# Performance work log

Measured on AMD Instinct MI355X. Metric: run time of the kernel, lower is better.

The kernel has to match this reference:

```python
import jax, jax.numpy as jnp
import numpy as np

B, H, VOCAB, STEPS = 256, 512, 100, 200  # TEXT_MAX_LEN - 1 = 200
SOS_IDX = 0  # char2idx['<SOS>'] == 0 (first entry of chars list)


def setup_inputs() -> dict:
    key = jax.random.key(0)
    ks = jax.random.split(key, 8)
    s = 0.05  # keep gates/tanh away from saturation, like trained-weight scale
    return {
        "feat": jax.random.normal(ks[0], (B, H), jnp.float32),          # resnet pooler_output
        "embed_table": jax.random.normal(ks[1], (VOCAB, H), jnp.float32) * s,
        "w_ih": jax.random.normal(ks[2], (3 * H, H), jnp.float32) * s,   # torch weight_ih_l0
        "w_hh": jax.random.normal(ks[3], (3 * H, H), jnp.float32) * s,   # torch weight_hh_l0
        "b_ih": jax.random.normal(ks[4], (3 * H,), jnp.float32) * s,
        "b_hh": jax.random.normal(ks[5], (3 * H,), jnp.float32) * s,
        "proj_w": jax.random.normal(ks[6], (VOCAB, H), jnp.float32) * s,
        "proj_b": jax.random.normal(ks[7], (VOCAB,), jnp.float32) * s,
    }


def _gru_cell(x, h, w_ih, w_hh, b_ih, b_hh):
    # torch GRU cell: gates ordered [r, z, n]
    gi = x @ w_ih.T + b_ih          # [B, 3H]
    gh = h @ w_hh.T + b_hh          # [B, 3H]
    i_r, i_z, i_n = jnp.split(gi, 3, axis=-1)
    h_r, h_z, h_n = jnp.split(gh, 3, axis=-1)
    r = jax.nn.sigmoid(i_r + h_r)
    z = jax.nn.sigmoid(i_z + h_z)
    n = jnp.tanh(i_n + r * h_n)
    return (1.0 - z) * n + z * h


def reference(feat, embed_table, w_ih, w_hh, b_ih, b_hh, proj_w, proj_b):
    batch = feat.shape[0]
    # hidden initialized from resnet features; first input = embed(<SOS>)
    h0 = feat                                             # [B, H]
    inp0 = jnp.broadcast_to(embed_table[SOS_IDX], (batch, H))

    def step(carry, _):
        inp, h = carry
        h_new = _gru_cell(inp, h, w_ih, w_hh, b_ih, b_hh)
        # GRU output == new hidden (1 layer); it is fed back as next input
        return (h_new, h_new), h_new

    _, outs = jax.lax.scan(step, (inp0, h0), None, length=STEPS)  # [T, B, H]
    res = jnp.transpose(outs, (1, 0, 2))                          # [B, T, H]
    logits = res @ proj_w.T + proj_b                              # [B, T, V]
    return jnp.transpose(logits, (0, 2, 1))                       # [B, V, T]
```

## Files before the change

kernel.cpp:

```cpp
#include <hip/hip_runtime.h>
#include <hip/hip_bf16.h>
#include <math.h>


typedef __bf16 bf16_t;
typedef __bf16 bf16x8 __attribute__((ext_vector_type(8)));
typedef float f32x4 __attribute__((ext_vector_type(4)));
typedef unsigned long long u64;
typedef unsigned short u16;

#define B_ 256
#define H_ 512
#define V_ 100
#define T_ 200
#define NF_ 131072
#define SLAB_ 24576
#define MFMA(a,b,c) __builtin_amdgcn_mfma_f32_16x16x32_bf16((a),(b),(c),0,0,0)

__device__ __forceinline__ float ld_in(const void* p, long i, int isf32) {
    return isf32 ? ((const float*)p)[i] : (float)((const bf16_t*)p)[i];
}

__device__ __forceinline__ bf16_t split_pick(double v, int sp) {
    bf16_t a = (bf16_t)(float)v;
    if (sp == 0) return a;
    double r1 = v - (double)(float)a;
    bf16_t b = (bf16_t)(float)r1;
    if (sp == 1) return b;
    double r2 = r1 - (double)(float)b;
    return (bf16_t)(float)r2;
}

union bfbits { __bf16 b; u16 u; };

__global__ __launch_bounds__(256) void convert_kernel(
    const void* __restrict__ feat, const void* __restrict__ embed,
    const void* __restrict__ wih,  const void* __restrict__ whh,
    const void* __restrict__ bih,  const void* __restrict__ bhh,
    const void* __restrict__ pw,   const void* __restrict__ pb,
    char* __restrict__ barr, int* __restrict__ flag,
    bf16_t* __restrict__ WB, bf16_t* __restrict__ W0, bf16_t* __restrict__ PB,
    bf16_t* __restrict__ hsp, double* __restrict__ hf,
    double* __restrict__ BB, double* __restrict__ pbd, double* __restrict__ gi0)
{
    __shared__ int s_cnt;
    if (threadIdx.x == 0) s_cnt = 0;
    __syncthreads();
    if (threadIdx.x < 128) {
        unsigned w = ((const unsigned*)feat)[threadIdx.x];
        unsigned e = (w >> 7) & 0xFFu;
        if (e >= 0x68u && e <= 0x85u) atomicAdd(&s_cnt, 1);
    }
    __syncthreads();
    const int isf32 = (s_cnt < 96) ? 1 : 0;
    if (blockIdx.x == 0) {
        if (threadIdx.x == 0) *flag = isf32;
        if (threadIdx.x < 256)
            *(int*)(barr + (size_t)threadIdx.x * 128) = 0;
        if (threadIdx.x < 8)
            *(int*)(barr + 32768 + (size_t)threadIdx.x * 128) = 0;
    }

    const long S0 = NF_;
    const long S1 = 3145728;
    const long S2 = 2359296;
    const long S3 = 114688;
    const long S4 = 2048;
    const long S5 = 100;
    const long S6 = 1536;
    const long TOT = S0 + S1 + S2 + S3 + S4 + S5 + S6;

    for (long g = blockIdx.x * 256L + threadIdx.x; g < TOT;
         g += (long)gridDim.x * 256L) {
        long i = g;
        if (i < S0) {
            double v = (double)ld_in(feat, i, isf32);
            hf[i] = v;
            hsp[i] = split_pick(v, 0);
            hsp[NF_ + i] = split_pick(v, 1);
            hsp[2 * NF_ + i] = split_pick(v, 2);
            continue;
        }
        i -= S0;
        if (i < S1) {
            long slab = i / SLAB_;  long rem = i % SLAB_;
            int grp = (int)(slab >> 5), jt = (int)(slab & 31);
            int sp = (int)(rem / 8192); long r2 = rem % 8192;
            int c = (int)(r2 / 512), r = (int)((r2 % 512) / 32), kk = (int)(r2 & 31);
            long n = jt * 16 + r, k = c * 32 + kk;
            double v;
            if (grp == 0)      v = (double)ld_in(wih, n * H_ + k, isf32) +
                                   (double)ld_in(whh, n * H_ + k, isf32);
            else if (grp == 1) v = (double)ld_in(wih, (512 + n) * H_ + k, isf32) +
                                   (double)ld_in(whh, (512 + n) * H_ + k, isf32);
            else if (grp == 2) v = (double)ld_in(wih, (1024 + n) * H_ + k, isf32);
            else               v = (double)ld_in(whh, (1024 + n) * H_ + k, isf32);
            WB[i] = split_pick(v, sp);
            continue;
        }
        i -= S1;
        if (i < S2) {
            long slab = i / SLAB_;  long rem = i % SLAB_;
            int grp = (int)(slab >> 5), jt = (int)(slab & 31);
            int sp = (int)(rem / 8192); long r2 = rem % 8192;
            int c = (int)(r2 / 512), r = (int)((r2 % 512) / 32), kk = (int)(r2 & 31);
            long n = jt * 16 + r, k = c * 32 + kk;
            long row = (grp == 0) ? n : (grp == 1) ? (512 + n) : (1024 + n);
            W0[i] = split_pick((double)ld_in(whh, row * H_ + k, isf32), sp);
            continue;
        }
        i -= S2;
        if (i < S3) {
            int vt = (int)(i / 16384); long rem = i % 16384;
            int sp = (int)(rem / 8192); long r2 = rem % 8192;
            int c = (int)(r2 / 512), r = (int)((r2 % 512) / 32), kk = (int)(r2 & 31);
            int v = vt * 16 + r;
            long k = c * 32 + kk;
            double val = (v < V_) ? (double)ld_in(pw, (long)v * H_ + k, isf32) : 0.0;
            PB[i] = split_pick(val, sp);
            continue;
        }
        i -= S3;
        if (i < S4) {
            int grp = (int)(i / 512), j = (int)(i & 511);
            double v;
            if (grp == 0)      v = (double)ld_in(bih, j, isf32) + (double)ld_in(bhh, j, isf32);
            else if (grp == 1) v = (double)ld_in(bih, 512 + j, isf32) + (double)ld_in(bhh, 512 + j, isf32);
            else if (grp == 2) v = (double)ld_in(bih, 1024 + j, isf32);
            else               v = (double)ld_in(bhh, 1024 + j, isf32);
            BB[i] = v;
            continue;
        }
        i -= S4;
        if (i < S5) { pbd[i] = (double)ld_in(pb, i, isf32); continue; }
        i -= S5;
        if (i < S6) {
            double acc = 0.0;
            #pragma unroll 8
            for (int k = 0; k < H_; ++k)
                acc += (double)ld_in(embed, k, isf32) *
                       (double)ld_in(wih, i * H_ + k, isf32);
            gi0[i] = acc;
        }
    }
}

#define WAITQ(N, s0, s1, s2, s3, s4, s5)                                   \
    asm volatile("s_waitcnt vmcnt(" #N ")"                                 \
                 : "+v"(s0), "+v"(s1), "+v"(s2), "+v"(s3), "+v"(s4),       \
                   "+v"(s5) :: "memory")

__global__ __launch_bounds__(512, 2) void gru_persist(
    const bf16_t* __restrict__ WB, const bf16_t* __restrict__ W0,
    const bf16_t* __restrict__ PB,
    bf16_t* __restrict__ hsp,
    const double* __restrict__ hf,
    const double* __restrict__ BB, const double* __restrict__ pbd,
    const double* __restrict__ gi0,
    const int* __restrict__ flag, char* __restrict__ barr,
    void* __restrict__ outp)
{
    __shared__ __align__(16) u64 Ad[2][3072];
    __shared__ double Gm[8][32][16];
    __shared__ __align__(16) bf16_t PBl[16384];
    __shared__ int s_slot;

    const int tid = threadIdx.x;
    const int w = tid >> 6;
    const int g = w & 3;
    const int par = w >> 2;
    const int lane = tid & 63;
    const int ln = lane & 15;
    const int quad = lane >> 4;

    unsigned xcc;
    asm volatile("s_getreg_b32 %0, hwreg(HW_REG_XCC_ID)" : "=s"(xcc));
    xcc &= 7u;
    if (tid == 0) {
        int* xslot = (int*)(barr + 32768 + (size_t)xcc * 128);
        s_slot = __hip_atomic_fetch_add(xslot, 1, __ATOMIC_RELAXED,
                                        __HIP_MEMORY_SCOPE_AGENT);
    }
    __syncthreads();
    const int jt = s_slot & 31;
    const int mh = (int)xcc;
    const int m0base = mh * 32;
    const int isf32 = *flag;

    int* const flagbase = (int*)(barr + (size_t)mh * 4096);
    int* const myflag   = flagbase + (size_t)jt * 32;
    int* const pollp    = flagbase + (size_t)(lane & 31) * 32;

    const int gm = tid >> 4;
    const int gj = tid & 15;
    const int jg = jt * 16 + gj;
    double hreg = hf[(long)(m0base + gm) * H_ + jg];
    const double bbR = BB[jg], bbZ = BB[512 + jg];
    const double bbNI = BB[1024 + jg], bbNH = BB[1536 + jg];
    const double g0R = gi0[jg], g0Z = gi0[512 + jg], g0NI = gi0[1024 + jg];

    bf16x8 Breg[8][3];
    {
        const int gg = (g == 3) ? 2 : g;
        const bf16_t* wpre = W0 + (long)(gg * 32 + jt) * SLAB_ + ln * 32 + quad * 8;
        #pragma unroll
        for (int n = 0; n < 8; ++n)
            #pragma unroll
            for (int sp = 0; sp < 3; ++sp)
                Breg[n][sp] = *(const bf16x8*)(wpre + sp * 8192 + (par + 2 * n) * 512);
    }
    const bf16_t* wpW = WB + (long)(g * 32 + jt) * SLAB_ + ln * 32 + quad * 8;

    const int tpj = jt & 1;

    if (jt < 14) {
        const bf16_t* src = PB + (long)(jt >> 1) * 16384;
        #pragma unroll
        for (int it = 0; it < 4; ++it) {
            int cg = it * 512 + tid;
            int h01 = cg >> 10, c = (cg >> 6) & 15, j = cg & 63;
            int L = (j & 3) * 16 + (j >> 2);
            *(bf16x8*)(PBl + h01 * 8192 + c * 512 + L * 8) =
                *(const bf16x8*)(src + cg * 8);
        }
    }

    const int lf = (((ln ^ quad) ^ ((ln & 1) << 2)) | (quad << 4)) * 8;

    int soff[6]; int ldst[6];
    #pragma unroll
    for (int i = 0; i < 6; ++i) {
        int u = i * 512 + tid;
        int sp = u >> 10, row = (u >> 5) & 31, k64 = u & 31;
        soff[i] = sp * 32768 + (m0base + row) * 128 + k64;
        int lc = k64 >> 3, qd = (k64 & 7) >> 1, half = k64 & 1;
        int lpos = (((row & 15) ^ qd) ^ ((row & 1) << 2)) | (qd << 4);
        ldst[i] = sp * 1024 + lc * 256 + (row >> 4) * 128 + lpos * 2 + half;
    }
    __syncthreads();

    for (int s = 0; s <= T_; ++s) {
        const u64* hin64 = (const u64*)(hsp + (long)(s & 1) * 3 * NF_);
        const bool gemm = (s < T_) && !(s == 0 && g == 2);
        const bool doproj = (s >= 1 && jt < 14 && w == (s & 7));

        double dg0[4] = {0, 0, 0, 0}, dg1[4] = {0, 0, 0, 0};
        f32x4 pacc = {0.f, 0.f, 0.f, 0.f};

        u64 sreg[24];
        #pragma unroll
        for (int qq = 0; qq < 4; ++qq)
            #pragma unroll
            for (int i = 0; i < 6; ++i) {
                const u64* p = hin64 + (long)soff[i] + qq * 32;
                asm volatile("global_load_dwordx2 %0, %1, off sc0"
                             : "=v"(sreg[qq * 6 + i]) : "v"(p));
            }

        WAITQ(18, sreg[0], sreg[1], sreg[2], sreg[3], sreg[4], sreg[5]);
        #pragma unroll
        for (int i = 0; i < 6; ++i) Ad[0][ldst[i]] = sreg[i];
        __syncthreads();

        #pragma unroll
        for (int q = 0; q < 4; ++q) {
            if (q < 3) {
                if (q == 0)
                    WAITQ(12, sreg[6], sreg[7], sreg[8], sreg[9], sreg[10], sreg[11]);
                else if (q == 1)
                    WAITQ(6, sreg[12], sreg[13], sreg[14], sreg[15], sreg[16], sreg[17]);
                else
                    WAITQ(0, sreg[18], sreg[19], sreg[20], sreg[21], sreg[22], sreg[23]);
                #pragma unroll
                for (int i = 0; i < 6; ++i)
                    Ad[(q + 1) & 1][ldst[i]] = sreg[(q + 1) * 6 + i];
            }
            const __bf16* Ab = (const __bf16*)(Ad[q & 1]);

            if (gemm) {
                #pragma unroll
                for (int t = 0; t < 2; ++t) {
                    const int lc = 2 * t + par;
                    const int n = 2 * q + t;
                    bf16x8 A0[3], A1[3];
                    #pragma unroll
                    for (int sp = 0; sp < 3; ++sp) {
                        A0[sp] = *(const bf16x8*)(Ab + sp * 4096 + lc * 1024 + lf);
                        A1[sp] = *(const bf16x8*)(Ab + sp * 4096 + lc * 1024 + 512 + lf);
                    }
                    f32x4 t0 = {0.f, 0.f, 0.f, 0.f};
                    t0 = MFMA(A0[0], Breg[n][2], t0);
                    t0 = MFMA(A0[1], Breg[n][1], t0);
                    t0 = MFMA(A0[2], Breg[n][0], t0);
                    t0 = MFMA(A0[0], Breg[n][1], t0);
                    t0 = MFMA(A0[1], Breg[n][0], t0);
                    t0 = MFMA(A0[0], Breg[n][0], t0);
                    f32x4 t1 = {0.f, 0.f, 0.f, 0.f};
                    t1 = MFMA(A1[0], Breg[n][2], t1);
                    t1 = MFMA(A1[1], Breg[n][1], t1);
                    t1 = MFMA(A1[2], Breg[n][0], t1);
                    t1 = MFMA(A1[0], Breg[n][1], t1);
                    t1 = MFMA(A1[1], Breg[n][0], t1);
                    t1 = MFMA(A1[0], Breg[n][0], t1);
                    #pragma unroll
                    for (int i = 0; i < 4; ++i) {
                        dg0[i] += (double)t0[i];
                        dg1[i] += (double)t1[i];
                    }
                }
            }
            if (doproj) {
                #pragma unroll
                for (int lc = 0; lc < 4; ++lc) {
                    const int c = q * 4 + lc;
                    bf16x8 pa1 = *(const bf16x8*)(Ab + 0 * 4096 + lc * 1024 + tpj * 512 + lf);
                    bf16x8 pa2 = *(const bf16x8*)(Ab + 1 * 4096 + lc * 1024 + tpj * 512 + lf);
                    bf16x8 b1v = *(const bf16x8*)(PBl + c * 512 + lane * 8);
                    bf16x8 b2v = *(const bf16x8*)(PBl + 8192 + c * 512 + lane * 8);
                    pacc = MFMA(pa1, b2v, pacc);
                    pacc = MFMA(pa2, b1v, pacc);
                    pacc = MFMA(pa1, b1v, pacc);
                }
            }
            if (q == 3 && s < T_) {
                #pragma unroll
                for (int i = 0; i < 4; ++i) {
                    Gm[w][quad * 4 + i][ln] = dg0[i];
                    Gm[w][16 + quad * 4 + i][ln] = dg1[i];
                }
            }
            __syncthreads();
        }

        if (doproj) {
            const int v = (jt >> 1) * 16 + ln;
            if (v < V_) {
                const double pbv = pbd[v];
                const int mtp = mh * 2 + tpj;
                #pragma unroll
                for (int i = 0; i < 4; ++i) {
                    const int m = mtp * 16 + quad * 4 + i;
                    const long idx = ((long)m * V_ + v) * T_ + (s - 1);
                    const float val = (float)((double)pacc[i] + pbv);
                    if (isf32) ((float*)outp)[idx] = val;
                    else       ((bf16_t*)outp)[idx] = (bf16_t)val;
                }
            }
        }

        if (s < T_) {
            {
                double R  = Gm[0][gm][gj] + Gm[4][gm][gj] + bbR;
                double Z  = Gm[1][gm][gj] + Gm[5][gm][gj] + bbZ;
                double NI = Gm[2][gm][gj] + Gm[6][gm][gj] + bbNI;
                double NH = Gm[3][gm][gj] + Gm[7][gm][gj] + bbNH;
                if (s == 0) { R += g0R; Z += g0Z; NI += g0NI; }
                const double r = 1.0 / (1.0 + exp(-R));
                const double z = 1.0 / (1.0 + exp(-Z));
                const double pre = NI + r * NH;
                const double n = 1.0 - 2.0 / (exp(2.0 * pre) + 1.0);
                hreg = (1.0 - z) * n + z * hreg;
                const long oi = (long)(m0base + gm) * H_ + jg;
                u16* ho = (u16*)(hsp + (long)((s + 1) & 1) * 3 * NF_);
                bfbits q1, q2, q3;
                q1.b = (bf16_t)(float)hreg;  double r1 = hreg - (double)(float)q1.b;
                q2.b = (bf16_t)(float)r1;    double r2 = r1 - (double)(float)q2.b;
                q3.b = (bf16_t)(float)r2;
                ho[oi] = q1.u;
                ho[NF_ + oi] = q2.u;
                ho[2 * NF_ + oi] = q3.u;
            }

            __syncthreads();
            if (tid == 0)
                __hip_atomic_store(myflag, s + 1, __ATOMIC_RELAXED,
                                   __HIP_MEMORY_SCOPE_AGENT);
            if (w == 0) {
                int lim = 0;
                for (;;) {
                    int v = (lane < 32)
                        ? __hip_atomic_load(pollp, __ATOMIC_RELAXED,
                                            __HIP_MEMORY_SCOPE_AGENT)
                        : 0x7fffffff;
                    if (__all(v >= s + 1)) break;
                    __builtin_amdgcn_s_sleep(1);
                    if (++lim > 100000000) break;
                }
            }
            __syncthreads();
            if (s == 0) {
                #pragma unroll
                for (int n = 0; n < 8; ++n)
                    #pragma unroll
                    for (int sp = 0; sp < 3; ++sp)
                        Breg[n][sp] = *(const bf16x8*)(wpW + sp * 8192 + (par + 2 * n) * 512);
            }
        }
    }
}

extern "C" void kernel_launch(void* const* d_in, const int* in_sizes, int n_in,
                              void* d_out, int out_size, void* d_ws, size_t ws_size,
                              hipStream_t stream) {
    char* ws = (char*)d_ws;
    char*   barr = ws;
    int*    flag = (int*)(ws + 40960);
    bf16_t* WB  = (bf16_t*)(ws + 41216);
    bf16_t* W0  = (bf16_t*)(ws + 6332672);
    bf16_t* PB  = (bf16_t*)(ws + 11051264);
    bf16_t* hsp = (bf16_t*)(ws + 11510016);
    double* hf  = (double*)(ws + 13082880);
    double* BB  = (double*)(ws + 14131456);
    double* pbd = (double*)(ws + 14147840);
    double* gi0 = (double*)(ws + 14148864);

    convert_kernel<<<1024, 256, 0, stream>>>(
        d_in[0], d_in[1], d_in[2], d_in[3], d_in[4], d_in[5], d_in[6], d_in[7],
        barr, flag, WB, W0, PB, hsp, hf, BB, pbd, gi0);

    gru_persist<<<256, 512, 0, stream>>>(
        WB, W0, PB, hsp, hf, BB, pbd, gi0, flag, barr, d_out);
}
```

Before: 1.460 ms.

## Poll inter-block flags from every wave and use 32-bit prep index math

In the persistent GRU kernel, every wave now spins on the inter-block step flags itself. This replaces the scheme where only wave 0 polled and a block-wide __syncthreads then released the others, and it is meant to cut one block barrier per timestep from the critical path. In exchange all waves now issue atomic flag loads, and all 64 lanes read pollp instead of only lanes below 32, which adds polling traffic and could read flags beyond the intended set. The weight-prep kernel also switches its index arithmetic from 64-bit to 32-bit to make the divisions and modulos cheaper.

```diff
diff --git a/kernel.cpp b/kernel.cpp
--- a/kernel.cpp
+++ b/kernel.cpp
@@ -8,6 +8,7 @@
 typedef float f32x4 __attribute__((ext_vector_type(4)));
 typedef unsigned long long u64;
 typedef unsigned short u16;
+typedef unsigned int u32;
 
 #define B_ 256
 #define H_ 512
@@ -61,18 +62,18 @@
             *(int*)(barr + 32768 + (size_t)threadIdx.x * 128) = 0;
     }
 
-    const long S0 = NF_;
-    const long S1 = 3145728;
-    const long S2 = 2359296;
-    const long S3 = 114688;
-    const long S4 = 2048;
-    const long S5 = 100;
-    const long S6 = 1536;
-    const long TOT = S0 + S1 + S2 + S3 + S4 + S5 + S6;
-
-    for (long g = blockIdx.x * 256L + threadIdx.x; g < TOT;
-         g += (long)gridDim.x * 256L) {
-        long i = g;
+    const u32 S0 = NF_;
+    const u32 S1 = 3145728;
+    const u32 S2 = 2359296;
+    const u32 S3 = 114688;
+    const u32 S4 = 2048;
+    const u32 S5 = 100;
+    const u32 S6 = 1536;
+    const u32 TOT = S0 + S1 + S2 + S3 + S4 + S5 + S6;
+
+    for (u32 g = blockIdx.x * 256u + threadIdx.x; g < TOT;
+         g += (u32)gridDim.x * 256u) {
+        u32 i = g;
         if (i < S0) {
             double v = (double)ld_in(feat, i, isf32);
             hf[i] = v;
@@ -83,11 +84,11 @@
         }
         i -= S0;
         if (i < S1) {
-            long slab = i / SLAB_;  long rem = i % SLAB_;
-            int grp = (int)(slab >> 5), jt = (int)(slab & 31);
-            int sp = (int)(rem / 8192); long r2 = rem % 8192;
-            int c = (int)(r2 / 512), r = (int)((r2 % 512) / 32), kk = (int)(r2 & 31);
-            long n = jt * 16 + r, k = c * 32 + kk;
+            u32 slab = i / SLAB_;  u32 rem = i % SLAB_;
+            u32 grp = slab >> 5, jt = slab & 31;
+            u32 sp = rem / 8192; u32 r2 = rem % 8192;
+            u32 c = r2 / 512, r = (r2 % 512) / 32, kk = r2 & 31;
+            u32 n = jt * 16 + r, k = c * 32 + kk;
             double v;
             if (grp == 0)      v = (double)ld_in(wih, n * H_ + k, isf32) +
                                    (double)ld_in(whh, n * H_ + k, isf32);
@@ -100,29 +101,29 @@
         }
         i -= S1;
         if (i < S2) {
-            long slab = i / SLAB_;  long rem = i % SLAB_;
-            int grp = (int)(slab >> 5), jt = (int)(slab & 31);
-            int sp = (int)(rem / 8192); long r2 = rem % 8192;
-            int c = (int)(r2 / 512), r = (int)((r2 % 512) / 32), kk = (int)(r2 & 31);
-            long n = jt * 16 + r, k = c * 32 + kk;
-            long row = (grp == 0) ? n : (grp == 1) ? (512 + n) : (1024 + n);
+            u32 slab = i / SLAB_;  u32 rem = i % SLAB_;
+            u32 grp = slab >> 5, jt = slab & 31;
+            u32 sp = rem / 8192; u32 r2 = rem % 8192;
+            u32 c = r2 / 512, r = (r2 % 512) / 32, kk = r2 & 31;
+            u32 n = jt * 16 + r, k = c * 32 + kk;
+            u32 row = (grp == 0) ? n : (grp == 1) ? (512 + n) : (1024 + n);
             W0[i] = split_pick((double)ld_in(whh, row * H_ + k, isf32), sp);
             continue;
         }
         i -= S2;
         if (i < S3) {
-            int vt = (int)(i / 16384); long rem = i % 16384;
-            int sp = (int)(rem / 8192); long r2 = rem % 8192;
-            int c = (int)(r2 / 512), r = (int)((r2 % 512) / 32), kk = (int)(r2 & 31);
-            int v = vt * 16 + r;
-            long k = c * 32 + kk;
-            double val = (v < V_) ? (double)ld_in(pw, (long)v * H_ + k, isf32) : 0.0;
+            u32 vt = i / 16384; u32 rem = i % 16384;
+            u32 sp = rem / 8192; u32 r2 = rem % 8192;
+            u32 c = r2 / 512, r = (r2 % 512) / 32, kk = r2 & 31;
+            u32 v = vt * 16 + r;
+            u32 k = c * 32 + kk;
+            double val = (v < V_) ? (double)ld_in(pw, (long)(v * H_ + k), isf32) : 0.0;
             PB[i] = split_pick(val, sp);
             continue;
         }
         i -= S3;
         if (i < S4) {
-            int grp = (int)(i / 512), j = (int)(i & 511);
+            u32 grp = i / 512, j = i & 511;
             double v;
             if (grp == 0)      v = (double)ld_in(bih, j, isf32) + (double)ld_in(bhh, j, isf32);
             else if (grp == 1) v = (double)ld_in(bih, 512 + j, isf32) + (double)ld_in(bhh, 512 + j, isf32);
@@ -137,7 +138,7 @@
         if (i < S6) {
             double acc = 0.0;
             #pragma unroll 8
-            for (int k = 0; k < H_; ++k)
+            for (u32 k = 0; k < H_; ++k)
                 acc += (double)ld_in(embed, k, isf32) *
                        (double)ld_in(wih, i * H_ + k, isf32);
             gi0[i] = acc;
@@ -375,19 +376,16 @@
             if (tid == 0)
                 __hip_atomic_store(myflag, s + 1, __ATOMIC_RELAXED,
                                    __HIP_MEMORY_SCOPE_AGENT);
-            if (w == 0) {
+            {
                 int lim = 0;
                 for (;;) {
-                    int v = (lane < 32)
-                        ? __hip_atomic_load(pollp, __ATOMIC_RELAXED,
-                                            __HIP_MEMORY_SCOPE_AGENT)
-                        : 0x7fffffff;
+                    int v = __hip_atomic_load(pollp, __ATOMIC_RELAXED,
+                                              __HIP_MEMORY_SCOPE_AGENT);
                     if (__all(v >= s + 1)) break;
                     __builtin_amdgcn_s_sleep(1);
                     if (++lim > 100000000) break;
                 }
             }
-            __syncthreads();
             if (s == 0) {
                 #pragma unroll
                 for (int n = 0; n < 8; ++n)
```

After: 1.485 ms. About the same (+1.8%).
